# Kernel tuning notes

Measured on AMD Instinct MI355X. Metric: run time of the kernel, lower is better.

Reference implementation:

```python
import jax, jax.numpy as jnp
import numpy as np

N = 100000
E = 1600000
F_IN = 128
HID = 128
EMB = 128
P_DROP = 0.1
NEG_SLOPE = 0.01  # torch leaky_relu default


def setup_inputs() -> dict:
    key = jax.random.key(0)
    ks = jax.random.split(key, 8)
    x = jax.random.normal(ks[0], (N, F_IN), dtype=jnp.float32)
    edge_index = jax.random.randint(ks[1], (2, E), 0, N, dtype=jnp.int64)
    s = 1.0 / np.sqrt(F_IN)
    W1 = jax.random.uniform(ks[2], (F_IN, HID), jnp.float32, -s, s)
    b1 = jnp.zeros((HID,), jnp.float32)
    s2 = 1.0 / np.sqrt(HID)
    W2 = jax.random.uniform(ks[3], (HID, EMB), jnp.float32, -s2, s2)
    b2 = jnp.zeros((EMB,), jnp.float32)
    s3 = 1.0 / np.sqrt(EMB)
    Wl = jax.random.uniform(ks[4], (EMB, 1), jnp.float32, -s3, s3)
    bl = jnp.zeros((1,), jnp.float32)
    return {"x": x, "edge_index": edge_index, "W1": W1, "b1": b1,
            "W2": W2, "b2": b2, "Wl": Wl, "bl": bl}


def _gcn_conv(x, W, b, src, dst, dinv_sqrt):
    # PyG GCNConv: h = x W; out = D^-1/2 (A + I) D^-1/2 h + b
    h = x @ W                                   # [N, F]
    norm = dinv_sqrt[src] * dinv_sqrt[dst]      # [E]
    agg = jax.ops.segment_sum(h[src] * norm[:, None], dst, num_segments=N)
    agg = agg + h * (dinv_sqrt * dinv_sqrt)[:, None]  # self-loop term
    return agg + b


def _dropout(x, key, p):
    keep = jax.random.bernoulli(key, 1.0 - p, x.shape)
    return jnp.where(keep, x / (1.0 - p), 0.0)


def reference(x, edge_index, W1, b1, W2, b2, Wl, bl):
    src, dst = edge_index[0], edge_index[1]
    # degree with self-loops (edge weight 1)
    deg = jax.ops.segment_sum(jnp.ones((E,), x.dtype), dst, num_segments=N) + 1.0
    dinv_sqrt = jax.lax.rsqrt(deg)

    dk1, dk2 = jax.random.split(jax.random.key(42))
    h = _gcn_conv(x, W1, b1, src, dst, dinv_sqrt)
    h = jax.nn.leaky_relu(h, NEG_SLOPE)
    h = _dropout(h, dk1, P_DROP)
    h = _gcn_conv(h, W2, b2, src, dst, dinv_sqrt)
    h = jax.nn.leaky_relu(h, NEG_SLOPE)
    h = _dropout(h, dk2, P_DROP)
    out = h @ Wl + bl                           # [N, 1]
    return out.reshape(-1)                      # [N]
```

## Files before the change

### kernel.cpp

```cpp
#include <hip/hip_runtime.h>
#include <hip/hip_fp16.h>
#include <stdint.h>

#define NN 100000
#define EE 1600000
#define FD 128
#define ELLCAP 64
#define NB 782
#define CHUNK 4096
#define NBLK 391
#define SMEM_BYTES 34816

typedef _Float16 half8 __attribute__((ext_vector_type(8)));
typedef float    floatx4 __attribute__((ext_vector_type(4)));

struct TF2 { uint32_t x0, x1; };

__host__ __device__ constexpr uint32_t rotl32c(uint32_t x, int d) {
  return (x << d) | (x >> (32 - d));
}

__host__ __device__ constexpr TF2 threefry2x32(uint32_t k0, uint32_t k1,
                                               uint32_t c0, uint32_t c1) {
  const uint32_t ks2 = k0 ^ k1 ^ 0x1BD11BDAu;
  uint32_t x0 = c0 + k0;
  uint32_t x1 = c1 + k1;
  const int r0[4] = {13, 15, 26, 6};
  const int r1[4] = {17, 29, 16, 24};
  for (int i = 0; i < 4; i++) { x0 += x1; x1 = rotl32c(x1, r0[i]); x1 ^= x0; }
  x0 += k1;  x1 += ks2 + 1u;
  for (int i = 0; i < 4; i++) { x0 += x1; x1 = rotl32c(x1, r1[i]); x1 ^= x0; }
  x0 += ks2; x1 += k0 + 2u;
  for (int i = 0; i < 4; i++) { x0 += x1; x1 = rotl32c(x1, r0[i]); x1 ^= x0; }
  x0 += k0;  x1 += k1 + 3u;
  for (int i = 0; i < 4; i++) { x0 += x1; x1 = rotl32c(x1, r1[i]); x1 ^= x0; }
  x0 += k1;  x1 += ks2 + 4u;
  for (int i = 0; i < 4; i++) { x0 += x1; x1 = rotl32c(x1, r0[i]); x1 ^= x0; }
  x0 += ks2; x1 += k0 + 5u;
  return TF2{x0, x1};
}

constexpr TF2 DK1 = threefry2x32(0u, 42u, 0u, 0u);
constexpr TF2 DK2 = threefry2x32(0u, 42u, 0u, 1u);

__device__ __forceinline__ float drop_scale(uint32_t k0, uint32_t k1, uint32_t m) {
  TF2 r = threefry2x32(k0, k1, 0u, m);
  const uint32_t bits = r.x0 ^ r.x1;
  float u = __uint_as_float((bits >> 9) | 0x3f800000u) - 1.0f;
  return (u < 0.9f) ? (1.0f / 0.9f) : 0.0f;
}

__device__ __forceinline__ void scatter_body(char* smem, int bid,
                                             const int* __restrict__ src,
                                             const int* __restrict__ dst,
                                             int* __restrict__ ebuf,
                                             unsigned* __restrict__ tcnt) {
  unsigned* sHist = (unsigned*)smem;
  unsigned* sScan = sHist + 1024;
  unsigned* sCur  = sScan + 1024;
  unsigned* sPart = sCur + 784;
  int*      sPay  = (int*)(sPart + 256);
  const int tid  = threadIdx.x;
  const int base = bid * CHUNK;

  for (int i = tid; i < 1024; i += 256) sHist[i] = 0u;
  __syncthreads();

#pragma unroll
  for (int j = 0; j < CHUNK / 256; ++j) {
    const int e = base + j * 256 + tid;
    if (e < EE) atomicAdd(&sHist[dst[e] >> 7], 1u);
  }
  __syncthreads();

  {
    const unsigned s0 = sHist[4 * tid + 0];
    const unsigned s1 = sHist[4 * tid + 1];
    const unsigned s2 = sHist[4 * tid + 2];
    const unsigned s3 = sHist[4 * tid + 3];
    sPart[tid] = s0 + s1 + s2 + s3;
    __syncthreads();
    for (int off = 1; off < 256; off <<= 1) {
      unsigned v = 0u;
      if (tid >= off) v = sPart[tid - off];
      __syncthreads();
      if (tid >= off) sPart[tid] += v;
      __syncthreads();
    }
    const unsigned excl = (tid == 0) ? 0u : sPart[tid - 1];
    sScan[4 * tid + 0] = excl;
    sScan[4 * tid + 1] = excl + s0;
    sScan[4 * tid + 2] = excl + s0 + s1;
    sScan[4 * tid + 3] = excl + s0 + s1 + s2;
  }
  for (int i = tid; i < NB; i += 256) sCur[i] = 0u;
  __syncthreads();

#pragma unroll
  for (int j = 0; j < CHUNK / 256; ++j) {
    const int e = base + j * 256 + tid;
    if (e < EE) {
      const int s = src[e];
      const int d = dst[e];
      const int b = d >> 7;
      const unsigned p = sScan[b] + atomicAdd(&sCur[b], 1u);
      sPay[p] = ((d & 127) << 17) | s;
    }
  }
  __syncthreads();

  {
    int4* g = (int4*)(ebuf + (size_t)bid * CHUNK);
    const int4* l = (const int4*)sPay;
#pragma unroll
    for (int i = tid; i < CHUNK / 4; i += 256) g[i] = l[i];
    for (int b = tid; b < NB; b += 256)
      tcnt[bid * 1024 + b] = (sScan[b] << 14) | sHist[b];
  }
}

template <typename IN>
__device__ __forceinline__ void gemm_body(char* smem, int bid,
                                          const IN* __restrict__ X,
                                          const float* __restrict__ W,
                                          __half* __restrict__ H) {
  _Float16 (*sWT)[136] = (_Float16(*)[136])smem;
  const int tid  = threadIdx.x;
  const int wave = tid >> 6;
  const int lane = tid & 63;
  const int quad = lane >> 4;
  const int m    = lane & 15;
  const int row0 = bid * 128;

  {
    const int n = tid & 127, g = tid >> 7;
#pragma unroll 4
    for (int j = 0; j < 32; ++j) {
      const int k = (g * 32 + j) * 2;
      union { _Float16 h[2]; uint32_t u; } p;
      p.h[0] = (_Float16)W[k * 128 + n];
      p.h[1] = (_Float16)W[(k + 1) * 128 + n];
      *(uint32_t*)&sWT[n][k] = p.u;
    }
  }
  __syncthreads();

  floatx4 acc[2][8];
#pragma unroll
  for (int rt = 0; rt < 2; ++rt)
#pragma unroll
    for (int ct = 0; ct < 8; ++ct) acc[rt][ct] = (floatx4){0.f, 0.f, 0.f, 0.f};

#pragma unroll
  for (int kk = 0; kk < 4; ++kk) {
    const int kb = kk * 32 + quad * 8;
    half8 a[2];
#pragma unroll
    for (int rt = 0; rt < 2; ++rt) {
      int gr = row0 + wave * 32 + rt * 16 + m;
      if (gr >= NN) gr = NN - 1;
      if constexpr (sizeof(IN) == 4) {
        const float4 lo = *(const float4*)(X + (size_t)gr * 128 + kb);
        const float4 hi = *(const float4*)(X + (size_t)gr * 128 + kb + 4);
        a[rt][0] = (_Float16)lo.x; a[rt][1] = (_Float16)lo.y;
        a[rt][2] = (_Float16)lo.z; a[rt][3] = (_Float16)lo.w;
        a[rt][4] = (_Float16)hi.x; a[rt][5] = (_Float16)hi.y;
        a[rt][6] = (_Float16)hi.z; a[rt][7] = (_Float16)hi.w;
      } else {
        a[rt] = *(const half8*)(X + (size_t)gr * 128 + kb);
      }
    }
#pragma unroll
    for (int ct = 0; ct < 8; ++ct) {
      const half8 b = *(const half8*)&sWT[ct * 16 + m][kb];
      acc[0][ct] = __builtin_amdgcn_mfma_f32_16x16x32_f16(a[0], b, acc[0][ct], 0, 0, 0);
      acc[1][ct] = __builtin_amdgcn_mfma_f32_16x16x32_f16(a[1], b, acc[1][ct], 0, 0, 0);
    }
  }

  __syncthreads();
#pragma unroll
  for (int rt = 0; rt < 2; ++rt)
#pragma unroll
    for (int reg = 0; reg < 4; ++reg) {
      const int row = wave * 32 + rt * 16 + quad * 4 + reg;
#pragma unroll
      for (int ct = 0; ct < 8; ++ct)
        sWT[row][ct * 16 + m] = (_Float16)acc[rt][ct][reg];
    }
  __syncthreads();
#pragma unroll
  for (int c = 0; c < 8; ++c) {
    const int chunk = tid + c * 256;
    const int row = chunk >> 4;
    const int seg = chunk & 15;
    const int gr = row0 + row;
    if (gr < NN)
      *(half8*)(H + (size_t)gr * 128 + seg * 8) =
          *(const half8*)&sWT[row][seg * 8];
  }
}

__global__ __launch_bounds__(256) void k_g1s(const float* __restrict__ X,
                                             const float* __restrict__ W,
                                             __half* __restrict__ H,
                                             const int* __restrict__ src,
                                             const int* __restrict__ dst,
                                             int* __restrict__ ebuf,
                                             unsigned* __restrict__ tcnt) {
  __shared__ __align__(16) char smem[SMEM_BYTES];
  if (blockIdx.x < NBLK) {
    scatter_body(smem, blockIdx.x, src, dst, ebuf, tcnt);
  } else {
    gemm_body<float>(smem, blockIdx.x - NBLK, X, W, H);
  }
}

__global__ __launch_bounds__(256) void k_build(const unsigned* __restrict__ tcnt,
                                               const int* __restrict__ ebuf,
                                               int* __restrict__ ell,
                                               unsigned* __restrict__ deg,
                                               float* __restrict__ dinv) {
  __shared__ int      sEll[128 * ELLCAP];
  __shared__ unsigned sFill[128];
  const int b   = blockIdx.x;
  const int tid = threadIdx.x;
  if (tid < 128) sFill[tid] = 0u;
  __syncthreads();

  for (int x = tid; x < NBLK; x += 256) {
    const unsigned t   = tcnt[x * 1024 + b];
    const unsigned off = t >> 14;
    const unsigned c   = t & 16383u;
    const int* p = ebuf + (size_t)x * CHUNK + off;
    for (unsigned i = 0; i < c; ++i) {
      const int pay = p[i];
      const int dl = (pay >> 17) & 127;
      const unsigned sl = atomicAdd(&sFill[dl], 1u);
      if (sl < ELLCAP) sEll[dl * ELLCAP + sl] = pay & 0x1FFFF;
    }
  }
  __syncthreads();

  const int node0 = b * 128;
  const int limRows = (NN - node0) < 128 ? (NN - node0) : 128;
  int4* g = (int4*)(ell + (size_t)node0 * ELLCAP);
  const int4* l = (const int4*)sEll;
  const int limV = limRows * (ELLCAP / 4);
  for (int i = tid; i < limV; i += 256) g[i] = l[i];
  if (tid < 128 && node0 + tid < NN) {
    const unsigned d = sFill[tid];
    deg[node0 + tid] = d;
    dinv[node0 + tid] = 1.0f / sqrtf((float)d + 1.0f);
  }
}

__global__ __launch_bounds__(256) void k_a1g2(const __half* __restrict__ H,
                                              const int* __restrict__ ell,
                                              const unsigned* __restrict__ degc,
                                              const float* __restrict__ dinv,
                                              const float* __restrict__ bias,
                                              const float* __restrict__ W2,
                                              __half* __restrict__ Hout) {
  __shared__ _Float16 sY[16][136];
  const int tid  = threadIdx.x;
  const int wave = tid >> 6;
  const int lane = tid & 63;
  const int quad = lane >> 4;
  const int ml   = lane & 15;
  const int row0 = blockIdx.x * 16;

  const __half2* __restrict__ H2 = (const __half2*)H;
  const char*    __restrict__ Hb = (const char*)H;
  const int coff = ml * 16;

  for (int j = 0; j < 4; ++j) {
    const int n = row0 + wave * 4 + j;
    const float di = dinv[n];

    unsigned cnt = degc[n];
    if (cnt > ELLCAP) cnt = ELLCAP;
    const int m = (int)cnt;
    int srcl = 0; float dl = 0.0f;
    if (lane < m) { srcl = ell[(size_t)n * ELLCAP + lane]; dl = dinv[srcl] * di; }
    const int wb = __float_as_int(dl);

    const uint32_t mb = (uint32_t)n * 128u + (uint32_t)lane * 2u;
    const float ds0 = drop_scale(DK1.x0, DK1.x1, mb + 0u);
    const float ds1 = drop_scale(DK1.x0, DK1.x1, mb + 1u);

    const float2 hv = __half22float2(H2[(size_t)n * 64 + lane]);
    const float sw = di * di;

    float acc[8];
#pragma unroll
    for (int r = 0; r < 8; ++r) acc[r] = 0.0f;

    for (int i = 0; i < m; i += 16) {
      int4 g[4];
#pragma unroll
      for (int k = 0; k < 4; ++k) {
        const int idx = i + 4 * k + quad;
        const unsigned s_ = (unsigned)__shfl(srcl, idx, 64);
        g[k] = *(const int4*)(Hb + (s_ * 256u + (unsigned)coff));
      }
      __builtin_amdgcn_sched_barrier(0);
#pragma unroll
      for (int k = 0; k < 4; ++k) {
        const int idx = i + 4 * k + quad;
        const float w_ = __int_as_float(__shfl(wb, idx, 64));
        const __half2* hp = (const __half2*)&g[k];
#pragma unroll
        for (int t = 0; t < 4; ++t) {
          const float2 f = __half22float2(hp[t]);
          acc[2 * t]     = fmaf(w_, f.x, acc[2 * t]);
          acc[2 * t + 1] = fmaf(w_, f.y, acc[2 * t + 1]);
        }
      }
    }

#pragma unroll
    for (int r = 0; r < 8; ++r) {
      acc[r] += __shfl_xor(acc[r], 16, 64);
      acc[r] += __shfl_xor(acc[r], 32, 64);
    }
    const int srcLane = lane >> 2;
    float b_[8];
#pragma unroll
    for (int r = 0; r < 8; ++r) b_[r] = __shfl(acc[r], srcLane, 64);
    const int t2 = lane & 3;
    float a0 = (t2 == 0) ? b_[0] : (t2 == 1) ? b_[2] : (t2 == 2) ? b_[4] : b_[6];
    float a1 = (t2 == 0) ? b_[1] : (t2 == 1) ? b_[3] : (t2 == 2) ? b_[5] : b_[7];
    a0 = fmaf(hv.x, sw, a0);
    a1 = fmaf(hv.y, sw, a1);

    const float2 b = ((const float2*)bias)[lane];
    float v0 = a0 + b.x, v1 = a1 + b.y;
    v0 = v0 >= 0.f ? v0 : 0.01f * v0;
    v1 = v1 >= 0.f ? v1 : 0.01f * v1;
    v0 *= ds0;
    v1 *= ds1;

    const int r = wave * 4 + j;
    sY[r][2 * lane]     = (_Float16)v0;
    sY[r][2 * lane + 1] = (_Float16)v1;
  }
  __syncthreads();

  floatx4 acc2[2];
  acc2[0] = (floatx4){0.f, 0.f, 0.f, 0.f};
  acc2[1] = (floatx4){0.f, 0.f, 0.f, 0.f};
#pragma unroll
  for (int kk = 0; kk < 4; ++kk) {
    const int kb = kk * 32 + quad * 8;
    const half8 a = *(const half8*)&sY[ml][kb];
#pragma unroll
    for (int t = 0; t < 2; ++t) {
      const int ct = wave * 2 + t;
      half8 bf;
#pragma unroll
      for (int i = 0; i < 8; ++i)
        bf[i] = (_Float16)W2[(size_t)(kb + i) * 128 + ct * 16 + ml];
      acc2[t] = __builtin_amdgcn_mfma_f32_16x16x32_f16(a, bf, acc2[t], 0, 0, 0);
    }
  }
  __syncthreads();

#pragma unroll
  for (int t = 0; t < 2; ++t)
#pragma unroll
    for (int reg = 0; reg < 4; ++reg)
      sY[quad * 4 + reg][(wave * 2 + t) * 16 + ml] = (_Float16)acc2[t][reg];
  __syncthreads();

  {
    const int row = tid >> 4;
    const int seg = tid & 15;
    *(half8*)(Hout + (size_t)(row0 + row) * 128 + seg * 8) =
        *(const half8*)&sY[row][seg * 8];
  }
}

template <int LAYER>
__global__ __launch_bounds__(256) void k_agg(const __half* __restrict__ H,
                                             const int* __restrict__ ell,
                                             const unsigned* __restrict__ degc,
                                             const float* __restrict__ dinv,
                                             const float* __restrict__ bias,
                                             const float* __restrict__ Wl,
                                             const float* __restrict__ bl,
                                             void* __restrict__ outv) {
  const int tid  = threadIdx.x;
  const int lane = tid & 63;
  const int n    = blockIdx.x * 4 + (tid >> 6);

  const float di = dinv[n];
  const __half2* __restrict__ H2 = (const __half2*)H;
  const char*    __restrict__ Hb = (const char*)H;

  unsigned cnt = degc[n];
  if (cnt > ELLCAP) cnt = ELLCAP;
  const int m = (int)cnt;
  int srcl = 0; float dl = 0.0f;
  if (lane < m) { srcl = ell[(size_t)n * ELLCAP + lane]; dl = dinv[srcl] * di; }
  const int wb = __float_as_int(dl);

  const uint32_t k0 = (LAYER == 1) ? DK1.x0 : DK2.x0;
  const uint32_t k1 = (LAYER == 1) ? DK1.x1 : DK2.x1;
  const uint32_t mb = (uint32_t)n * 128u + (uint32_t)lane * 2u;
  const float ds0 = drop_scale(k0, k1, mb + 0u);
  const float ds1 = drop_scale(k0, k1, mb + 1u);

  const float2 hv = __half22float2(H2[(size_t)n * 64 + lane]);
  const float sw = di * di;

  const int q    = lane >> 4;
  const int coff = (lane & 15) * 16;

  float acc[8];
#pragma unroll
  for (int r = 0; r < 8; ++r) acc[r] = 0.0f;

  for (int i = 0; i < m; i += 16) {
    int4 g[4];
#pragma unroll
    for (int k = 0; k < 4; ++k) {
      const int idx = i + 4 * k + q;
      const unsigned s_ = (unsigned)__shfl(srcl, idx, 64);
      g[k] = *(const int4*)(Hb + (s_ * 256u + (unsigned)coff));
    }
    __builtin_amdgcn_sched_barrier(0);
#pragma unroll
    for (int k = 0; k < 4; ++k) {
      const int idx = i + 4 * k + q;
      const float w_ = __int_as_float(__shfl(wb, idx, 64));
      const __half2* hp = (const __half2*)&g[k];
#pragma unroll
      for (int t = 0; t < 4; ++t) {
        const float2 f = __half22float2(hp[t]);
        acc[2 * t]     = fmaf(w_, f.x, acc[2 * t]);
        acc[2 * t + 1] = fmaf(w_, f.y, acc[2 * t + 1]);
      }
    }
  }

#pragma unroll
  for (int r = 0; r < 8; ++r) {
    acc[r] += __shfl_xor(acc[r], 16, 64);
    acc[r] += __shfl_xor(acc[r], 32, 64);
  }
  const int srcLane = lane >> 2;
  float b_[8];
#pragma unroll
  for (int r = 0; r < 8; ++r) b_[r] = __shfl(acc[r], srcLane, 64);
  const int t2 = lane & 3;
  float a0 = (t2 == 0) ? b_[0] : (t2 == 1) ? b_[2] : (t2 == 2) ? b_[4] : b_[6];
  float a1 = (t2 == 0) ? b_[1] : (t2 == 1) ? b_[3] : (t2 == 2) ? b_[5] : b_[7];
  a0 = fmaf(hv.x, sw, a0);
  a1 = fmaf(hv.y, sw, a1);

  const float2 b = ((const float2*)bias)[lane];
  float v0 = a0 + b.x, v1 = a1 + b.y;
  v0 = v0 >= 0.f ? v0 : 0.01f * v0;
  v1 = v1 >= 0.f ? v1 : 0.01f * v1;

  v0 *= ds0;
  v1 *= ds1;

  if constexpr (LAYER == 1) {
    __half2* out = (__half2*)outv;
    out[(size_t)n * 64 + lane] = __floats2half2_rn(v0, v1);
  } else {
    float* out = (float*)outv;
    const float2 wl = ((const float2*)Wl)[lane];
    float p = v0 * wl.x + v1 * wl.y;
#pragma unroll
    for (int d = 32; d > 0; d >>= 1) p += __shfl_down(p, d, 64);
    if (lane == 0) out[n] = p + bl[0];
  }
}

extern "C" void kernel_launch(void* const* d_in, const int* in_sizes, int n_in,
                              void* d_out, int out_size, void* d_ws, size_t ws_size,
                              hipStream_t stream) {
  const float* x  = (const float*)d_in[0];
  const int*   ei = (const int*)d_in[1];
  const float* W1 = (const float*)d_in[2];
  const float* b1 = (const float*)d_in[3];
  const float* W2 = (const float*)d_in[4];
  const float* b2 = (const float*)d_in[5];
  const float* Wl = (const float*)d_in[6];
  const float* bl = (const float*)d_in[7];
  float* out = (float*)d_out;

  unsigned* deg  = (unsigned*)d_ws;
  float*    dinv = (float*)(deg + NN);
  int*      ell  = (int*)(dinv + NN);
  __half*   bufA = (__half*)(ell + (size_t)NN * ELLCAP);
  __half*   bufB = bufA + (size_t)NN * FD;
  int*      ebuf = (int*)bufB;
  unsigned* tcnt = (unsigned*)(ebuf + (size_t)NBLK * CHUNK);

  const int* srcI = ei;
  const int* dstI = ei + EE;

  const int gemmGrid = (NN + 127) / 128;
  k_g1s<<<NBLK + gemmGrid, 256, 0, stream>>>(x, W1, bufA, srcI, dstI,
                                             ebuf, tcnt);
  k_build<<<NB, 256, 0, stream>>>(tcnt, ebuf, ell, deg, dinv);
  k_a1g2<<<NN / 16, 256, 0, stream>>>(bufA, ell, deg, dinv,
                                      b1, W2, bufB);
  k_agg<2><<<NN / 4, 256, 0, stream>>>(bufB, ell, deg, dinv,
                                       b2, Wl, bl, out);
}
```

Before: 282.4 us.

## Make each wave own 16 rows in fused layer-1 aggregate + W2 GEMM

Each wave now aggregates 16 nodes and runs the full 16x128 MFMA tile for its own rows in a private shared-memory slice. This removes all block-level __syncthreads and cuts the grid fourfold. Each block covers 64 rows, so per-block W2 loads are spread over more rows. The cost is more accumulator registers per wave (8 floatx4), which may lower occupancy, and W2 is still re-read from global per wave. It also packs the half2 shared stores and adds bounds clamping for the non-multiple row count.

```diff
diff --git a/kernel.cpp b/kernel.cpp
--- a/kernel.cpp
+++ b/kernel.cpp
@@ -262,20 +262,21 @@
                                               const float* __restrict__ bias,
                                               const float* __restrict__ W2,
                                               __half* __restrict__ Hout) {
-  __shared__ _Float16 sY[16][136];
+  __shared__ __align__(16) _Float16 sY[4][16][136];
   const int tid  = threadIdx.x;
   const int wave = tid >> 6;
   const int lane = tid & 63;
   const int quad = lane >> 4;
   const int ml   = lane & 15;
-  const int row0 = blockIdx.x * 16;
+  const int nb   = blockIdx.x * 64 + wave * 16;
 
   const __half2* __restrict__ H2 = (const __half2*)H;
   const char*    __restrict__ Hb = (const char*)H;
   const int coff = ml * 16;
 
-  for (int j = 0; j < 4; ++j) {
-    const int n = row0 + wave * 4 + j;
+  for (int j = 0; j < 16; ++j) {
+    int n = nb + j;
+    if (n >= NN) n = NN - 1;
     const float di = dinv[n];
 
     unsigned cnt = degc[n];
@@ -341,43 +342,43 @@
     v0 *= ds0;
     v1 *= ds1;
 
-    const int r = wave * 4 + j;
-    sY[r][2 * lane]     = (_Float16)v0;
-    sY[r][2 * lane + 1] = (_Float16)v1;
-  }
-  __syncthreads();
-
-  floatx4 acc2[2];
-  acc2[0] = (floatx4){0.f, 0.f, 0.f, 0.f};
-  acc2[1] = (floatx4){0.f, 0.f, 0.f, 0.f};
+    union { _Float16 h[2]; uint32_t u; } p;
+    p.h[0] = (_Float16)v0; p.h[1] = (_Float16)v1;
+    *(uint32_t*)&sY[wave][j][2 * lane] = p.u;
+  }
+
+  floatx4 acc2[8];
+#pragma unroll
+  for (int ct = 0; ct < 8; ++ct) acc2[ct] = (floatx4){0.f, 0.f, 0.f, 0.f};
 #pragma unroll
   for (int kk = 0; kk < 4; ++kk) {
     const int kb = kk * 32 + quad * 8;
-    const half8 a = *(const half8*)&sY[ml][kb];
-#pragma unroll
-    for (int t = 0; t < 2; ++t) {
-      const int ct = wave * 2 + t;
+    const half8 a = *(const half8*)&sY[wave][ml][kb];
+#pragma unroll
+    for (int ct = 0; ct < 8; ++ct) {
       half8 bf;
 #pragma unroll
       for (int i = 0; i < 8; ++i)
         bf[i] = (_Float16)W2[(size_t)(kb + i) * 128 + ct * 16 + ml];
-      acc2[t] = __builtin_amdgcn_mfma_f32_16x16x32_f16(a, bf, acc2[t], 0, 0, 0);
-    }
-  }
-  __syncthreads();
-
-#pragma unroll
-  for (int t = 0; t < 2; ++t)
+      acc2[ct] = __builtin_amdgcn_mfma_f32_16x16x32_f16(a, bf, acc2[ct], 0, 0, 0);
+    }
+  }
+
+#pragma unroll
+  for (int ct = 0; ct < 8; ++ct)
 #pragma unroll
     for (int reg = 0; reg < 4; ++reg)
-      sY[quad * 4 + reg][(wave * 2 + t) * 16 + ml] = (_Float16)acc2[t][reg];
-  __syncthreads();
-
-  {
-    const int row = tid >> 4;
-    const int seg = tid & 15;
-    *(half8*)(Hout + (size_t)(row0 + row) * 128 + seg * 8) =
-        *(const half8*)&sY[row][seg * 8];
+      sY[wave][quad * 4 + reg][ct * 16 + ml] = (_Float16)acc2[ct][reg];
+
+#pragma unroll
+  for (int c = 0; c < 4; ++c) {
+    const int chunk = lane + c * 64;
+    const int row = chunk >> 4;
+    const int seg = chunk & 15;
+    const int gr = nb + row;
+    if (gr < NN)
+      *(half8*)(Hout + (size_t)gr * 128 + seg * 8) =
+          *(const half8*)&sY[wave][row][seg * 8];
   }
 }
 
@@ -508,8 +509,8 @@
   k_g1s<<<NBLK + gemmGrid, 256, 0, stream>>>(x, W1, bufA, srcI, dstI,
                                              ebuf, tcnt);
   k_build<<<NB, 256, 0, stream>>>(tcnt, ebuf, ell, deg, dinv);
-  k_a1g2<<<NN / 16, 256, 0, stream>>>(bufA, ell, deg, dinv,
-                                      b1, W2, bufB);
+  k_a1g2<<<(NN + 63) / 64, 256, 0, stream>>>(bufA, ell, deg, dinv,
+                                             b1, W2, bufB);
   k_agg<2><<<NN / 4, 256, 0, stream>>>(bufB, ell, deg, dinv,
                                        b2, Wl, bl, out);
 }
```

New measurement: 320.0 us. 13.3% more time.

## Replace two-pass bucketed ELL build with direct global-atomic fill

Applied to the files above, without the earlier changes.

Drops the shared-memory histogram/scan scatter and the separate k_build kernel. The ELL adjacency is now filled directly with global atomicAdd on per-node degree counters, after a memset. dinv is no longer stored; each consumer recomputes it from the degree. This removes a kernel launch and the ebuf round trip, at the cost of about 1.6M contended global atomics with scattered writes. Neighbour order within a row becomes nondeterministic, which can change floating-point summation order.

```diff
diff --git a/kernel.cpp b/kernel.cpp
--- a/kernel.cpp
+++ b/kernel.cpp
@@ -6,7 +6,6 @@
 #define EE 1600000
 #define FD 128
 #define ELLCAP 64
-#define NB 782
 #define CHUNK 4096
 #define NBLK 391
 #define SMEM_BYTES 34816
@@ -50,72 +49,27 @@
   return (u < 0.9f) ? (1.0f / 0.9f) : 0.0f;
 }
 
-__device__ __forceinline__ void scatter_body(char* smem, int bid,
-                                             const int* __restrict__ src,
-                                             const int* __restrict__ dst,
-                                             int* __restrict__ ebuf,
-                                             unsigned* __restrict__ tcnt) {
-  unsigned* sHist = (unsigned*)smem;
-  unsigned* sScan = sHist + 1024;
-  unsigned* sCur  = sScan + 1024;
-  unsigned* sPart = sCur + 784;
-  int*      sPay  = (int*)(sPart + 256);
-  const int tid  = threadIdx.x;
-  const int base = bid * CHUNK;
-
-  for (int i = tid; i < 1024; i += 256) sHist[i] = 0u;
-  __syncthreads();
-
-#pragma unroll
-  for (int j = 0; j < CHUNK / 256; ++j) {
-    const int e = base + j * 256 + tid;
-    if (e < EE) atomicAdd(&sHist[dst[e] >> 7], 1u);
-  }
-  __syncthreads();
-
-  {
-    const unsigned s0 = sHist[4 * tid + 0];
-    const unsigned s1 = sHist[4 * tid + 1];
-    const unsigned s2 = sHist[4 * tid + 2];
-    const unsigned s3 = sHist[4 * tid + 3];
-    sPart[tid] = s0 + s1 + s2 + s3;
-    __syncthreads();
-    for (int off = 1; off < 256; off <<= 1) {
-      unsigned v = 0u;
-      if (tid >= off) v = sPart[tid - off];
-      __syncthreads();
-      if (tid >= off) sPart[tid] += v;
-      __syncthreads();
-    }
-    const unsigned excl = (tid == 0) ? 0u : sPart[tid - 1];
-    sScan[4 * tid + 0] = excl;
-    sScan[4 * tid + 1] = excl + s0;
-    sScan[4 * tid + 2] = excl + s0 + s1;
-    sScan[4 * tid + 3] = excl + s0 + s1 + s2;
-  }
-  for (int i = tid; i < NB; i += 256) sCur[i] = 0u;
-  __syncthreads();
-
-#pragma unroll
-  for (int j = 0; j < CHUNK / 256; ++j) {
-    const int e = base + j * 256 + tid;
+__device__ __forceinline__ void fill_body(int bid,
+                                          const int* __restrict__ src,
+                                          const int* __restrict__ dst,
+                                          int* __restrict__ ell,
+                                          unsigned* __restrict__ deg) {
+  const int tid = threadIdx.x;
+#pragma unroll
+  for (int j = 0; j < CHUNK / 1024; ++j) {
+    const int e = bid * CHUNK + j * 1024 + tid * 4;
     if (e < EE) {
-      const int s = src[e];
-      const int d = dst[e];
-      const int b = d >> 7;
-      const unsigned p = sScan[b] + atomicAdd(&sCur[b], 1u);
-      sPay[p] = ((d & 127) << 17) | s;
-    }
-  }
-  __syncthreads();
-
-  {
-    int4* g = (int4*)(ebuf + (size_t)bid * CHUNK);
-    const int4* l = (const int4*)sPay;
-#pragma unroll
-    for (int i = tid; i < CHUNK / 4; i += 256) g[i] = l[i];
-    for (int b = tid; b < NB; b += 256)
-      tcnt[bid * 1024 + b] = (sScan[b] << 14) | sHist[b];
+      const int4 s4 = *(const int4*)(src + e);
+      const int4 d4 = *(const int4*)(dst + e);
+      const unsigned sl0 = atomicAdd(&deg[d4.x], 1u);
+      const unsigned sl1 = atomicAdd(&deg[d4.y], 1u);
+      const unsigned sl2 = atomicAdd(&deg[d4.z], 1u);
+      const unsigned sl3 = atomicAdd(&deg[d4.w], 1u);
+      if (sl0 < ELLCAP) ell[(size_t)d4.x * ELLCAP + sl0] = s4.x;
+      if (sl1 < ELLCAP) ell[(size_t)d4.y * ELLCAP + sl1] = s4.y;
+      if (sl2 < ELLCAP) ell[(size_t)d4.z * ELLCAP + sl2] = s4.z;
+      if (sl3 < ELLCAP) ell[(size_t)d4.w * ELLCAP + sl3] = s4.w;
+    }
   }
 }
 
@@ -206,59 +160,19 @@
                                              __half* __restrict__ H,
                                              const int* __restrict__ src,
                                              const int* __restrict__ dst,
-                                             int* __restrict__ ebuf,
-                                             unsigned* __restrict__ tcnt) {
+                                             int* __restrict__ ell,
+                                             unsigned* __restrict__ deg) {
   __shared__ __align__(16) char smem[SMEM_BYTES];
   if (blockIdx.x < NBLK) {
-    scatter_body(smem, blockIdx.x, src, dst, ebuf, tcnt);
+    fill_body(blockIdx.x, src, dst, ell, deg);
   } else {
     gemm_body<float>(smem, blockIdx.x - NBLK, X, W, H);
-  }
-}
-
-__global__ __launch_bounds__(256) void k_build(const unsigned* __restrict__ tcnt,
-                                               const int* __restrict__ ebuf,
-                                               int* __restrict__ ell,
-                                               unsigned* __restrict__ deg,
-                                               float* __restrict__ dinv) {
-  __shared__ int      sEll[128 * ELLCAP];
-  __shared__ unsigned sFill[128];
-  const int b   = blockIdx.x;
-  const int tid = threadIdx.x;
-  if (tid < 128) sFill[tid] = 0u;
-  __syncthreads();
-
-  for (int x = tid; x < NBLK; x += 256) {
-    const unsigned t   = tcnt[x * 1024 + b];
-    const unsigned off = t >> 14;
-    const unsigned c   = t & 16383u;
-    const int* p = ebuf + (size_t)x * CHUNK + off;
-    for (unsigned i = 0; i < c; ++i) {
-      const int pay = p[i];
-      const int dl = (pay >> 17) & 127;
-      const unsigned sl = atomicAdd(&sFill[dl], 1u);
-      if (sl < ELLCAP) sEll[dl * ELLCAP + sl] = pay & 0x1FFFF;
-    }
-  }
-  __syncthreads();
-
-  const int node0 = b * 128;
-  const int limRows = (NN - node0) < 128 ? (NN - node0) : 128;
-  int4* g = (int4*)(ell + (size_t)node0 * ELLCAP);
-  const int4* l = (const int4*)sEll;
-  const int limV = limRows * (ELLCAP / 4);
-  for (int i = tid; i < limV; i += 256) g[i] = l[i];
-  if (tid < 128 && node0 + tid < NN) {
-    const unsigned d = sFill[tid];
-    deg[node0 + tid] = d;
-    dinv[node0 + tid] = 1.0f / sqrtf((float)d + 1.0f);
   }
 }
 
 __global__ __launch_bounds__(256) void k_a1g2(const __half* __restrict__ H,
                                               const int* __restrict__ ell,
                                               const unsigned* __restrict__ degc,
-                                              const float* __restrict__ dinv,
                                               const float* __restrict__ bias,
                                               const float* __restrict__ W2,
                                               __half* __restrict__ Hout) {
@@ -276,13 +190,17 @@
 
   for (int j = 0; j < 4; ++j) {
     const int n = row0 + wave * 4 + j;
-    const float di = dinv[n];
-
-    unsigned cnt = degc[n];
+    const unsigned d0 = degc[n];
+    const float di = 1.0f / sqrtf((float)d0 + 1.0f);
+
+    unsigned cnt = d0;
     if (cnt > ELLCAP) cnt = ELLCAP;
     const int m = (int)cnt;
     int srcl = 0; float dl = 0.0f;
-    if (lane < m) { srcl = ell[(size_t)n * ELLCAP + lane]; dl = dinv[srcl] * di; }
+    if (lane < m) {
+      srcl = ell[(size_t)n * ELLCAP + lane];
+      dl = (1.0f / sqrtf((float)degc[srcl] + 1.0f)) * di;
+    }
     const int wb = __float_as_int(dl);
 
     const uint32_t mb = (uint32_t)n * 128u + (uint32_t)lane * 2u;
@@ -385,7 +303,6 @@
 __global__ __launch_bounds__(256) void k_agg(const __half* __restrict__ H,
                                              const int* __restrict__ ell,
                                              const unsigned* __restrict__ degc,
-                                             const float* __restrict__ dinv,
                                              const float* __restrict__ bias,
                                              const float* __restrict__ Wl,
                                              const float* __restrict__ bl,
@@ -394,15 +311,19 @@
   const int lane = tid & 63;
   const int n    = blockIdx.x * 4 + (tid >> 6);
 
-  const float di = dinv[n];
   const __half2* __restrict__ H2 = (const __half2*)H;
   const char*    __restrict__ Hb = (const char*)H;
 
-  unsigned cnt = degc[n];
+  const unsigned d0 = degc[n];
+  const float di = 1.0f / sqrtf((float)d0 + 1.0f);
+  unsigned cnt = d0;
   if (cnt > ELLCAP) cnt = ELLCAP;
   const int m = (int)cnt;
   int srcl = 0; float dl = 0.0f;
-  if (lane < m) { srcl = ell[(size_t)n * ELLCAP + lane]; dl = dinv[srcl] * di; }
+  if (lane < m) {
+    srcl = ell[(size_t)n * ELLCAP + lane];
+    dl = (1.0f / sqrtf((float)degc[srcl] + 1.0f)) * di;
+  }
   const int wb = __float_as_int(dl);
 
   const uint32_t k0 = (LAYER == 1) ? DK1.x0 : DK2.x0;
@@ -494,22 +415,18 @@
   float* out = (float*)d_out;
 
   unsigned* deg  = (unsigned*)d_ws;
-  float*    dinv = (float*)(deg + NN);
-  int*      ell  = (int*)(dinv + NN);
+  int*      ell  = (int*)(deg + NN);
   __half*   bufA = (__half*)(ell + (size_t)NN * ELLCAP);
   __half*   bufB = bufA + (size_t)NN * FD;
-  int*      ebuf = (int*)bufB;
-  unsigned* tcnt = (unsigned*)(ebuf + (size_t)NBLK * CHUNK);
 
   const int* srcI = ei;
   const int* dstI = ei + EE;
 
+  hipMemsetAsync(deg, 0, NN * sizeof(unsigned), stream);
+
   const int gemmGrid = (NN + 127) / 128;
   k_g1s<<<NBLK + gemmGrid, 256, 0, stream>>>(x, W1, bufA, srcI, dstI,
-                                             ebuf, tcnt);
-  k_build<<<NB, 256, 0, stream>>>(tcnt, ebuf, ell, deg, dinv);
-  k_a1g2<<<NN / 16, 256, 0, stream>>>(bufA, ell, deg, dinv,
-                                      b1, W2, bufB);
-  k_agg<2><<<NN / 4, 256, 0, stream>>>(bufB, ell, deg, dinv,
-                                       b2, Wl, bl, out);
-}
+                                             ell, deg);
+  k_a1g2<<<NN / 16, 256, 0, stream>>>(bufA, ell, deg, b1, W2, bufB);
+  k_agg<2><<<NN / 4, 256, 0, stream>>>(bufB, ell, deg, b2, Wl, bl, out);
+}
```

Result: slower. 371.9 us (+31.7%).
